# Performance work log

Measured on AMD Instinct MI355X. Metric: run time of the kernel, lower is better.

Reference implementation:

```python
import jax, jax.numpy as jnp
import numpy as np
from jax import lax

T, B, V, N = 128, 256, 256, 1024


def setup_inputs() -> dict:
    key = jax.random.key(0)
    k1, k2, k3, k4 = jax.random.split(key, 4)
    inputs = jax.random.uniform(k1, (T, B, V), dtype=jnp.float32)
    labels = jax.random.uniform(k2, (T * B, V), dtype=jnp.float32)
    weights = jax.random.normal(k3, (V + N, N), dtype=jnp.float32) * 0.1
    bias = jnp.zeros((N,), dtype=jnp.float32)
    output_weights = jax.random.normal(k4, (N, V), dtype=jnp.float32) * 0.1
    output_bias = jnp.zeros((V,), dtype=jnp.float32)
    return {
        "inputs": inputs,
        "labels": labels,
        "weights": weights,
        "bias": bias,
        "output_weights": output_weights,
        "output_bias": output_bias,
    }


def reference(inputs, labels, weights, bias, output_weights, output_bias):
    t, b, v = inputs.shape
    n = weights.shape[1]
    # split concat-matmul into x@Wx + h@Wh (same math as concat([x,h]) @ W)
    w_x = weights[:v]   # [V, N]
    w_h = weights[v:]   # [N, N]

    def step(h, x):
        h_new = jnp.tanh(x @ w_x + h @ w_h + bias)
        return h_new, h_new

    h0 = jnp.zeros((b, n), dtype=inputs.dtype)
    _, outputs = lax.scan(step, h0, inputs)          # [T, B, N]
    outputs = outputs.reshape(t * b, n)              # concat over time
    logits = outputs @ output_weights + output_bias  # [T*B, V]
    # softmax_cross_entropy_with_logits (soft labels), then mean
    log_p = jax.nn.log_softmax(logits, axis=-1)
    loss = jnp.mean(-jnp.sum(labels * log_p, axis=-1))
    return loss
```

## Files before the change

kernel.cpp:

```cpp
#include <hip/hip_runtime.h>
#include <math.h>

typedef __bf16 bf16;
typedef __attribute__((ext_vector_type(4))) __bf16 bf16x4;
typedef __attribute__((ext_vector_type(8))) __bf16 bf16x8;
typedef __attribute__((ext_vector_type(4))) float f32x4;

#define T_STEPS 128
#define B_SZ    256
#define V_SZ    256
#define N_SZ    1024
#define NROWS   (T_STEPS * B_SZ)
#define RSTR    68
#define LSTR    17
#define NGRP    16
#define NCB     16

__device__ __forceinline__ float fast_tanh(float x) {
    float e = __expf(2.0f * x);
    return 1.0f - 2.0f / (e + 1.0f);
}

__global__ void k_convert(const float* __restrict__ src, bf16* __restrict__ dst, int n) {
    int i = (blockIdx.x * blockDim.x + threadIdx.x) * 4;
    if (i < n) {
        float4 v = *(const float4*)(src + i);
        bf16x4 o;
        o.x = (bf16)v.x; o.y = (bf16)v.y; o.z = (bf16)v.z; o.w = (bf16)v.w;
        *(bf16x4*)(dst + i) = o;
    }
}

__global__ void k_transpose_cvt(const float* __restrict__ src, bf16* __restrict__ dst,
                                int R, int C) {
    __shared__ float tile[32][33];
    int c0 = blockIdx.x * 32;
    int r0 = blockIdx.y * 32;
    int tx = threadIdx.x & 31;
    int ty = threadIdx.x >> 5;
#pragma unroll
    for (int i = 0; i < 32; i += 8)
        tile[ty + i][tx] = src[(size_t)(r0 + ty + i) * C + c0 + tx];
    __syncthreads();
#pragma unroll
    for (int i = 0; i < 32; i += 8)
        dst[(size_t)(c0 + ty + i) * R + r0 + tx] = (bf16)tile[tx][ty + i];
}

__global__ __launch_bounds__(512, 2) void k_rnn(
    const bf16* __restrict__ Xb,
    const bf16* __restrict__ Wxt,
    const bf16* __restrict__ Wht,
    const bf16* __restrict__ Wot,
    const float* __restrict__ bias,
    bf16* __restrict__ XH,
    unsigned int* __restrict__ Lgu,
    int* __restrict__ cnt)
{
    __shared__ float red[8 * 16 * RSTR];
    __shared__ float lred[8 * 16 * LSTR];
    const int tid  = threadIdx.x;
    const int lane = tid & 63;
    const int w    = tid >> 6;
    const int quad = lane >> 4;
    const int l15  = lane & 15;
    const int g  = blockIdx.x >> 4;
    const int c  = blockIdx.x & 15;
    const int m0 = g * 16;
    const int n0 = c * 64;
    const int k0 = w * 128;
    const int v0 = w * 32;
    int* gcnt = cnt + g * T_STEPS;

    const bf16* Bp = Wht + (size_t)(n0 + l15) * N_SZ + k0 + quad * 8;
    bf16x8 b[4][4];
#pragma unroll
    for (int nt = 0; nt < 4; ++nt)
#pragma unroll
        for (int kc = 0; kc < 4; ++kc)
            b[nt][kc] = *(const bf16x8*)&Bp[(size_t)(nt * 16) * N_SZ + kc * 32];
    bf16x8 bx[4];
#pragma unroll
    for (int nt = 0; nt < 4; ++nt)
        bx[nt] = *(const bf16x8*)&Wxt[(size_t)(n0 + nt * 16 + l15) * V_SZ + v0 + quad * 8];
    bf16x8 bo[4];
#pragma unroll
    for (int kc = 0; kc < 4; ++kc)
        bo[kc] = *(const bf16x8*)&Wot[(size_t)(c * 16 + l15) * N_SZ + k0 + kc * 32 + quad * 8];

    const int orow = tid >> 5;
    const int ocol = (tid & 31) * 2;
    const float bias0 = bias[n0 + ocol];
    const float bias1 = bias[n0 + ocol + 1];
    const int lrow = w * 2 + (lane >> 3);
    const int lvp  = lane & 7;
    unsigned int* XHu = (unsigned int*)XH;
    const f32x4 zz = {0.f, 0.f, 0.f, 0.f};

    {
        bf16x8 ax = *(const bf16x8*)&Xb[(size_t)(m0 + l15) * V_SZ + v0 + quad * 8];
        f32x4 acc[4] = {zz, zz, zz, zz};
#pragma unroll
        for (int nt = 0; nt < 4; ++nt)
            acc[nt] = __builtin_amdgcn_mfma_f32_16x16x32_bf16(ax, bx[nt], acc[nt], 0, 0, 0);
#pragma unroll
        for (int nt = 0; nt < 4; ++nt)
#pragma unroll
            for (int r = 0; r < 4; ++r)
                red[(w * 16 + quad * 4 + r) * RSTR + nt * 16 + l15] = acc[nt][r];
        __syncthreads();
        float s0 = bias0, s1 = bias1;
#pragma unroll
        for (int w2 = 0; w2 < 8; ++w2) {
            float2 v = *(const float2*)&red[(w2 * 16 + orow) * RSTR + ocol];
            s0 += v.x; s1 += v.y;
        }
        bf16 r0 = (bf16)fast_tanh(s0);
        bf16 r1 = (bf16)fast_tanh(s1);
        unsigned int outw = (unsigned int)__builtin_bit_cast(unsigned short, r0)
                          | ((unsigned int)__builtin_bit_cast(unsigned short, r1) << 16);
        size_t oidx = (((size_t)0 * B_SZ + m0 + orow) * N_SZ + n0 + ocol) >> 1;
        __hip_atomic_store(&XHu[oidx], outw, __ATOMIC_RELAXED, __HIP_MEMORY_SCOPE_AGENT);
        asm volatile("s_waitcnt vmcnt(0)" ::: "memory");
        __syncthreads();
        if (tid == 0)
            __hip_atomic_fetch_add(&gcnt[0], 1, __ATOMIC_RELAXED, __HIP_MEMORY_SCOPE_AGENT);
    }

    for (int t = 1; t < T_STEPS; ++t) {
        bf16x8 ax = *(const bf16x8*)&Xb[((size_t)t * B_SZ + m0 + l15) * V_SZ + v0 + quad * 8];

        if (tid == 0) {
            while (__hip_atomic_load(&gcnt[t - 1], __ATOMIC_RELAXED,
                                     __HIP_MEMORY_SCOPE_AGENT) < NCB)
                __builtin_amdgcn_s_sleep(1);
        }
        __syncthreads();

        const bf16* Ap = XH + ((size_t)(t - 1) * B_SZ + m0 + l15) * N_SZ + k0 + quad * 8;
        bf16x8 a[4];
#pragma unroll
        for (int kc = 0; kc < 4; ++kc)
            a[kc] = *(const bf16x8*)&Ap[kc * 32];

        f32x4 acc[4] = {zz, zz, zz, zz};
#pragma unroll
        for (int nt = 0; nt < 4; ++nt)
            acc[nt] = __builtin_amdgcn_mfma_f32_16x16x32_bf16(ax, bx[nt], acc[nt], 0, 0, 0);
#pragma unroll
        for (int kc = 0; kc < 4; ++kc)
#pragma unroll
            for (int nt = 0; nt < 4; ++nt)
                acc[nt] = __builtin_amdgcn_mfma_f32_16x16x32_bf16(a[kc], b[nt][kc],
                                                                  acc[nt], 0, 0, 0);
        f32x4 lacc = zz;
#pragma unroll
        for (int kc = 0; kc < 4; ++kc)
            lacc = __builtin_amdgcn_mfma_f32_16x16x32_bf16(a[kc], bo[kc], lacc, 0, 0, 0);

#pragma unroll
        for (int nt = 0; nt < 4; ++nt)
#pragma unroll
            for (int r = 0; r < 4; ++r)
                red[(w * 16 + quad * 4 + r) * RSTR + nt * 16 + l15] = acc[nt][r];
#pragma unroll
        for (int r = 0; r < 4; ++r)
            lred[(w * 16 + quad * 4 + r) * LSTR + l15] = lacc[r];
        __syncthreads();

        float s0 = bias0, s1 = bias1;
#pragma unroll
        for (int w2 = 0; w2 < 8; ++w2) {
            float2 v = *(const float2*)&red[(w2 * 16 + orow) * RSTR + ocol];
            s0 += v.x; s1 += v.y;
        }
        bf16 r0 = (bf16)fast_tanh(s0);
        bf16 r1 = (bf16)fast_tanh(s1);
        unsigned int outw = (unsigned int)__builtin_bit_cast(unsigned short, r0)
                          | ((unsigned int)__builtin_bit_cast(unsigned short, r1) << 16);
        size_t oidx = (((size_t)t * B_SZ + m0 + orow) * N_SZ + n0 + ocol) >> 1;
        __hip_atomic_store(&XHu[oidx], outw, __ATOMIC_RELAXED, __HIP_MEMORY_SCOPE_AGENT);

        if (lane < 16) {
            float sa = 0.f, sb = 0.f;
#pragma unroll
            for (int w2 = 0; w2 < 8; ++w2) {
                sa += lred[(w2 * 16 + lrow) * LSTR + lvp * 2];
                sb += lred[(w2 * 16 + lrow) * LSTR + lvp * 2 + 1];
            }
            bf16 pa = (bf16)sa, pb = (bf16)sb;
            unsigned int pw = (unsigned int)__builtin_bit_cast(unsigned short, pa)
                            | ((unsigned int)__builtin_bit_cast(unsigned short, pb) << 16);
            Lgu[(((size_t)(t - 1) * 16 + c) * B_SZ + m0 + lrow) * 8 + lvp] = pw;
        }

        asm volatile("s_waitcnt vmcnt(0)" ::: "memory");
        __syncthreads();
        if (tid == 0)
            __hip_atomic_fetch_add(&gcnt[t], 1, __ATOMIC_RELAXED, __HIP_MEMORY_SCOPE_AGENT);
    }

    if (tid == 0) {
        while (__hip_atomic_load(&gcnt[T_STEPS - 1], __ATOMIC_RELAXED,
                                 __HIP_MEMORY_SCOPE_AGENT) < NCB)
            __builtin_amdgcn_s_sleep(1);
    }
    __syncthreads();
    {
        const bf16* Ap = XH + ((size_t)(T_STEPS - 1) * B_SZ + m0 + l15) * N_SZ + k0 + quad * 8;
        bf16x8 a[4];
#pragma unroll
        for (int kc = 0; kc < 4; ++kc)
            a[kc] = *(const bf16x8*)&Ap[kc * 32];
        f32x4 lacc = zz;
#pragma unroll
        for (int kc = 0; kc < 4; ++kc)
            lacc = __builtin_amdgcn_mfma_f32_16x16x32_bf16(a[kc], bo[kc], lacc, 0, 0, 0);
#pragma unroll
        for (int r = 0; r < 4; ++r)
            lred[(w * 16 + quad * 4 + r) * LSTR + l15] = lacc[r];
        __syncthreads();
        if (lane < 16) {
            float sa = 0.f, sb = 0.f;
#pragma unroll
            for (int w2 = 0; w2 < 8; ++w2) {
                sa += lred[(w2 * 16 + lrow) * LSTR + lvp * 2];
                sb += lred[(w2 * 16 + lrow) * LSTR + lvp * 2 + 1];
            }
            bf16 pa = (bf16)sa, pb = (bf16)sb;
            unsigned int pw = (unsigned int)__builtin_bit_cast(unsigned short, pa)
                            | ((unsigned int)__builtin_bit_cast(unsigned short, pb) << 16);
            Lgu[(((size_t)(T_STEPS - 1) * 16 + c) * B_SZ + m0 + lrow) * 8 + lvp] = pw;
        }
    }
}

__global__ __launch_bounds__(256) void k_lred(
    const bf16* __restrict__ Lg,
    const float* __restrict__ labels,
    const float* __restrict__ ob,
    float* __restrict__ out)
{
    __shared__ float bt[4];
    const int tid  = threadIdx.x;
    const int lane = tid & 63;
    const int w    = tid >> 6;
    const int cs   = lane >> 2;
    const int vi   = (lane & 3) * 4;
    const float4 ob4 = *(const float4*)&ob[cs * 16 + vi];

    float wtot = 0.f;
    for (int i = 0; i < 32; ++i) {
        int row  = blockIdx.x * 128 + w * 32 + i;
        int p    = row >> 8;
        int brow = row & 255;
        bf16x4 lv = *(const bf16x4*)&Lg[(((size_t)p * 16 + cs) * B_SZ + brow) * 16 + vi];
        float l0 = (float)lv.x + ob4.x;
        float l1 = (float)lv.y + ob4.y;
        float l2 = (float)lv.z + ob4.z;
        float l3 = (float)lv.w + ob4.w;
        float mx = fmaxf(fmaxf(l0, l1), fmaxf(l2, l3));
#pragma unroll
        for (int s = 1; s < 64; s <<= 1)
            mx = fmaxf(mx, __shfl_xor(mx, s, 64));
        float sume = __expf(l0 - mx) + __expf(l1 - mx) + __expf(l2 - mx) + __expf(l3 - mx);
        const float4 lb = *(const float4*)&labels[(size_t)row * V_SZ + cs * 16 + vi];
        float labs = lb.x + lb.y + lb.z + lb.w;
        float labv = lb.x * l0 + lb.y * l1 + lb.z * l2 + lb.w * l3;
#pragma unroll
        for (int s = 1; s < 64; s <<= 1) {
            sume += __shfl_xor(sume, s, 64);
            labs += __shfl_xor(labs, s, 64);
            labv += __shfl_xor(labv, s, 64);
        }
        float lse = mx + __logf(sume);
        wtot += labs * lse - labv;
    }
    if (lane == 0) bt[w] = wtot;
    __syncthreads();
    if (tid == 0)
        atomicAdd(out, (bt[0] + bt[1] + bt[2] + bt[3]) * (1.0f / (float)NROWS));
}

extern "C" void kernel_launch(void* const* d_in, const int* in_sizes, int n_in,
                              void* d_out, int out_size, void* d_ws, size_t ws_size,
                              hipStream_t stream)
{
    const float* inputs  = (const float*)d_in[0];
    const float* labels  = (const float*)d_in[1];
    const float* weights = (const float*)d_in[2];
    const float* bias    = (const float*)d_in[3];
    const float* out_w   = (const float*)d_in[4];
    const float* out_b   = (const float*)d_in[5];
    float* out = (float*)d_out;

    char* ws = (char*)d_ws;
    bf16* XH  = (bf16*)ws;  ws += (size_t)NROWS * N_SZ * 2;
    bf16* Xb  = (bf16*)ws;  ws += (size_t)NROWS * V_SZ * 2;
    bf16* Lg  = (bf16*)ws;  ws += (size_t)NROWS * V_SZ * 2;
    bf16* Wxt = (bf16*)ws;  ws += (size_t)N_SZ * V_SZ * 2;
    bf16* Wht = (bf16*)ws;  ws += (size_t)N_SZ * N_SZ * 2;
    bf16* Wot = (bf16*)ws;  ws += (size_t)V_SZ * N_SZ * 2;
    int*  cnt = (int*)ws;   ws += (size_t)NGRP * T_STEPS * 4;

    hipMemsetAsync(out, 0, sizeof(float), stream);
    hipMemsetAsync(cnt, 0, (size_t)NGRP * T_STEPS * 4, stream);

    k_convert<<<dim3(NROWS * V_SZ / 1024), 256, 0, stream>>>(inputs, Xb, NROWS * V_SZ);
    k_transpose_cvt<<<dim3(N_SZ / 32, V_SZ / 32), 256, 0, stream>>>(weights, Wxt, V_SZ, N_SZ);
    k_transpose_cvt<<<dim3(N_SZ / 32, N_SZ / 32), 256, 0, stream>>>(
        weights + (size_t)V_SZ * N_SZ, Wht, N_SZ, N_SZ);
    k_transpose_cvt<<<dim3(V_SZ / 32, N_SZ / 32), 256, 0, stream>>>(out_w, Wot, N_SZ, V_SZ);

    k_rnn<<<dim3(NGRP * NCB), 512, 0, stream>>>(Xb, Wxt, Wht, Wot, bias, XH,
                                                (unsigned int*)Lg, cnt);

    k_lred<<<dim3(NROWS / 128), 256, 0, stream>>>(Lg, labels, out_b, out);
}
```

Measured before the change: 504.0 us.

## Repartition RNN blocks to pair batch groups with narrower column slices

Each block now handles two 16-row batch groups and a 32-column slice of the hidden state, which halves the recurrent weight registers per block while keeping 256 blocks. The output-projection work is split between two half-blocks, and each half writes a partial logit buffer that the loss kernel sums. The wait on the previous step moves to the end of each iteration, so the loss-partial reduction overlaps the spin. In exchange each block now waits on two counters with 32 arrivals each, and the workspace for logits doubles.

```diff
diff --git a/kernel.cpp b/kernel.cpp
--- a/kernel.cpp
+++ b/kernel.cpp
@@ -11,10 +11,10 @@
 #define V_SZ    256
 #define N_SZ    1024
 #define NROWS   (T_STEPS * B_SZ)
-#define RSTR    68
-#define LSTR    17
+#define RST     36
+#define LST     17
 #define NGRP    16
-#define NCB     16
+#define NCB2    32
 
 __device__ __forceinline__ float fast_tanh(float x) {
     float e = __expf(2.0f * x);
@@ -57,181 +57,197 @@
     unsigned int* __restrict__ Lgu,
     int* __restrict__ cnt)
 {
-    __shared__ float red[8 * 16 * RSTR];
-    __shared__ float lred[8 * 16 * LSTR];
+    __shared__ float red0[8 * 16 * RST];
+    __shared__ float red1[8 * 16 * RST];
+    __shared__ float lred0[4 * 16 * LST];
+    __shared__ float lred1[4 * 16 * LST];
     const int tid  = threadIdx.x;
     const int lane = tid & 63;
     const int w    = tid >> 6;
     const int quad = lane >> 4;
     const int l15  = lane & 15;
-    const int g  = blockIdx.x >> 4;
-    const int c  = blockIdx.x & 15;
-    const int m0 = g * 16;
-    const int n0 = c * 64;
+    const int gp = blockIdx.x >> 5;
+    const int c  = blockIdx.x & 31;
+    const int g0 = gp * 2, g1 = gp * 2 + 1;
+    const int m00 = g0 * 16, m01 = g1 * 16;
+    const int n0 = c * 32;
     const int k0 = w * 128;
     const int v0 = w * 32;
-    int* gcnt = cnt + g * T_STEPS;
+    const int h  = c & 1;
+    const int s  = c >> 1;
+    const bool lossw = ((w >> 2) == h);
+    const int wl = w & 3;
+    int* gc0 = cnt + g0 * T_STEPS;
+    int* gc1 = cnt + g1 * T_STEPS;
 
     const bf16* Bp = Wht + (size_t)(n0 + l15) * N_SZ + k0 + quad * 8;
-    bf16x8 b[4][4];
-#pragma unroll
-    for (int nt = 0; nt < 4; ++nt)
+    bf16x8 b[2][4];
+#pragma unroll
+    for (int nt = 0; nt < 2; ++nt)
 #pragma unroll
         for (int kc = 0; kc < 4; ++kc)
             b[nt][kc] = *(const bf16x8*)&Bp[(size_t)(nt * 16) * N_SZ + kc * 32];
-    bf16x8 bx[4];
-#pragma unroll
-    for (int nt = 0; nt < 4; ++nt)
+    bf16x8 bx[2];
+#pragma unroll
+    for (int nt = 0; nt < 2; ++nt)
         bx[nt] = *(const bf16x8*)&Wxt[(size_t)(n0 + nt * 16 + l15) * V_SZ + v0 + quad * 8];
     bf16x8 bo[4];
-#pragma unroll
-    for (int kc = 0; kc < 4; ++kc)
-        bo[kc] = *(const bf16x8*)&Wot[(size_t)(c * 16 + l15) * N_SZ + k0 + kc * 32 + quad * 8];
-
-    const int orow = tid >> 5;
-    const int ocol = (tid & 31) * 2;
+    if (lossw) {
+#pragma unroll
+        for (int kc = 0; kc < 4; ++kc)
+            bo[kc] = *(const bf16x8*)&Wot[(size_t)(s * 16 + l15) * N_SZ + k0 + kc * 32 + quad * 8];
+    }
+
+    const int  et   = tid & 255;
+    const int  orow = et >> 4;
+    const int  ocol = (et & 15) * 2;
+    const int  mg   = (tid >= 256) ? m01 : m00;
+    float* redp = (tid >= 256) ? red1 : red0;
     const float bias0 = bias[n0 + ocol];
     const float bias1 = bias[n0 + ocol + 1];
-    const int lrow = w * 2 + (lane >> 3);
-    const int lvp  = lane & 7;
+    const bool lactive = (tid >= 128 && tid < 256) || (tid >= 384);
+    const int  lt   = (tid >= 384) ? (tid - 384) : (tid - 128);
+    const int  lrow = lt >> 3, lvp = lt & 7;
+    float* lredp = (tid >= 384) ? lred1 : lred0;
+    const int  lm  = (tid >= 384) ? m01 : m00;
     unsigned int* XHu = (unsigned int*)XH;
     const f32x4 zz = {0.f, 0.f, 0.f, 0.f};
 
     {
-        bf16x8 ax = *(const bf16x8*)&Xb[(size_t)(m0 + l15) * V_SZ + v0 + quad * 8];
-        f32x4 acc[4] = {zz, zz, zz, zz};
-#pragma unroll
-        for (int nt = 0; nt < 4; ++nt)
-            acc[nt] = __builtin_amdgcn_mfma_f32_16x16x32_bf16(ax, bx[nt], acc[nt], 0, 0, 0);
-#pragma unroll
-        for (int nt = 0; nt < 4; ++nt)
-#pragma unroll
-            for (int r = 0; r < 4; ++r)
-                red[(w * 16 + quad * 4 + r) * RSTR + nt * 16 + l15] = acc[nt][r];
+        bf16x8 ax0 = *(const bf16x8*)&Xb[(size_t)(m00 + l15) * V_SZ + v0 + quad * 8];
+        bf16x8 ax1 = *(const bf16x8*)&Xb[(size_t)(m01 + l15) * V_SZ + v0 + quad * 8];
+        f32x4 acc0[2] = {zz, zz}, acc1[2] = {zz, zz};
+#pragma unroll
+        for (int nt = 0; nt < 2; ++nt) {
+            acc0[nt] = __builtin_amdgcn_mfma_f32_16x16x32_bf16(ax0, bx[nt], acc0[nt], 0, 0, 0);
+            acc1[nt] = __builtin_amdgcn_mfma_f32_16x16x32_bf16(ax1, bx[nt], acc1[nt], 0, 0, 0);
+        }
+#pragma unroll
+        for (int nt = 0; nt < 2; ++nt)
+#pragma unroll
+            for (int r = 0; r < 4; ++r) {
+                red0[(w * 16 + quad * 4 + r) * RST + nt * 16 + l15] = acc0[nt][r];
+                red1[(w * 16 + quad * 4 + r) * RST + nt * 16 + l15] = acc1[nt][r];
+            }
         __syncthreads();
         float s0 = bias0, s1 = bias1;
 #pragma unroll
         for (int w2 = 0; w2 < 8; ++w2) {
-            float2 v = *(const float2*)&red[(w2 * 16 + orow) * RSTR + ocol];
+            float2 v = *(const float2*)&redp[(w2 * 16 + orow) * RST + ocol];
             s0 += v.x; s1 += v.y;
         }
         bf16 r0 = (bf16)fast_tanh(s0);
         bf16 r1 = (bf16)fast_tanh(s1);
         unsigned int outw = (unsigned int)__builtin_bit_cast(unsigned short, r0)
                           | ((unsigned int)__builtin_bit_cast(unsigned short, r1) << 16);
-        size_t oidx = (((size_t)0 * B_SZ + m0 + orow) * N_SZ + n0 + ocol) >> 1;
+        size_t oidx = (((size_t)mg + orow) * N_SZ + n0 + ocol) >> 1;
         __hip_atomic_store(&XHu[oidx], outw, __ATOMIC_RELAXED, __HIP_MEMORY_SCOPE_AGENT);
         asm volatile("s_waitcnt vmcnt(0)" ::: "memory");
         __syncthreads();
-        if (tid == 0)
-            __hip_atomic_fetch_add(&gcnt[0], 1, __ATOMIC_RELAXED, __HIP_MEMORY_SCOPE_AGENT);
-    }
-
-    for (int t = 1; t < T_STEPS; ++t) {
-        bf16x8 ax = *(const bf16x8*)&Xb[((size_t)t * B_SZ + m0 + l15) * V_SZ + v0 + quad * 8];
-
         if (tid == 0) {
-            while (__hip_atomic_load(&gcnt[t - 1], __ATOMIC_RELAXED,
-                                     __HIP_MEMORY_SCOPE_AGENT) < NCB)
+            __hip_atomic_fetch_add(&gc0[0], 1, __ATOMIC_RELAXED, __HIP_MEMORY_SCOPE_AGENT);
+            __hip_atomic_fetch_add(&gc1[0], 1, __ATOMIC_RELAXED, __HIP_MEMORY_SCOPE_AGENT);
+            while (__hip_atomic_load(&gc0[0], __ATOMIC_RELAXED, __HIP_MEMORY_SCOPE_AGENT) < NCB2)
                 __builtin_amdgcn_s_sleep(1);
-        }
-        __syncthreads();
-
-        const bf16* Ap = XH + ((size_t)(t - 1) * B_SZ + m0 + l15) * N_SZ + k0 + quad * 8;
-        bf16x8 a[4];
-#pragma unroll
-        for (int kc = 0; kc < 4; ++kc)
-            a[kc] = *(const bf16x8*)&Ap[kc * 32];
-
-        f32x4 acc[4] = {zz, zz, zz, zz};
-#pragma unroll
-        for (int nt = 0; nt < 4; ++nt)
-            acc[nt] = __builtin_amdgcn_mfma_f32_16x16x32_bf16(ax, bx[nt], acc[nt], 0, 0, 0);
-#pragma unroll
-        for (int kc = 0; kc < 4; ++kc)
-#pragma unroll
-            for (int nt = 0; nt < 4; ++nt)
-                acc[nt] = __builtin_amdgcn_mfma_f32_16x16x32_bf16(a[kc], b[nt][kc],
-                                                                  acc[nt], 0, 0, 0);
-        f32x4 lacc = zz;
-#pragma unroll
-        for (int kc = 0; kc < 4; ++kc)
-            lacc = __builtin_amdgcn_mfma_f32_16x16x32_bf16(a[kc], bo[kc], lacc, 0, 0, 0);
-
-#pragma unroll
-        for (int nt = 0; nt < 4; ++nt)
-#pragma unroll
-            for (int r = 0; r < 4; ++r)
-                red[(w * 16 + quad * 4 + r) * RSTR + nt * 16 + l15] = acc[nt][r];
-#pragma unroll
-        for (int r = 0; r < 4; ++r)
-            lred[(w * 16 + quad * 4 + r) * LSTR + l15] = lacc[r];
-        __syncthreads();
-
-        float s0 = bias0, s1 = bias1;
-#pragma unroll
-        for (int w2 = 0; w2 < 8; ++w2) {
-            float2 v = *(const float2*)&red[(w2 * 16 + orow) * RSTR + ocol];
-            s0 += v.x; s1 += v.y;
-        }
-        bf16 r0 = (bf16)fast_tanh(s0);
-        bf16 r1 = (bf16)fast_tanh(s1);
-        unsigned int outw = (unsigned int)__builtin_bit_cast(unsigned short, r0)
-                          | ((unsigned int)__builtin_bit_cast(unsigned short, r1) << 16);
-        size_t oidx = (((size_t)t * B_SZ + m0 + orow) * N_SZ + n0 + ocol) >> 1;
-        __hip_atomic_store(&XHu[oidx], outw, __ATOMIC_RELAXED, __HIP_MEMORY_SCOPE_AGENT);
-
-        if (lane < 16) {
+            while (__hip_atomic_load(&gc1[0], __ATOMIC_RELAXED, __HIP_MEMORY_SCOPE_AGENT) < NCB2)
+                __builtin_amdgcn_s_sleep(1);
+        }
+        __syncthreads();
+    }
+
+    for (int t = 1; t <= T_STEPS; ++t) {
+        const bool do_step = (t < T_STEPS);
+
+        bf16x8 ax0, ax1;
+        if (do_step) {
+            ax0 = *(const bf16x8*)&Xb[((size_t)t * B_SZ + m00 + l15) * V_SZ + v0 + quad * 8];
+            ax1 = *(const bf16x8*)&Xb[((size_t)t * B_SZ + m01 + l15) * V_SZ + v0 + quad * 8];
+        }
+
+        const bf16* Ap0 = XH + ((size_t)(t - 1) * B_SZ + m00 + l15) * N_SZ + k0 + quad * 8;
+        const bf16* Ap1 = XH + ((size_t)(t - 1) * B_SZ + m01 + l15) * N_SZ + k0 + quad * 8;
+        bf16x8 a0[4], a1[4];
+#pragma unroll
+        for (int kc = 0; kc < 4; ++kc) {
+            a0[kc] = *(const bf16x8*)&Ap0[kc * 32];
+            a1[kc] = *(const bf16x8*)&Ap1[kc * 32];
+        }
+
+        if (do_step) {
+            f32x4 acc0[2] = {zz, zz}, acc1[2] = {zz, zz};
+#pragma unroll
+            for (int nt = 0; nt < 2; ++nt) {
+                acc0[nt] = __builtin_amdgcn_mfma_f32_16x16x32_bf16(ax0, bx[nt], acc0[nt], 0, 0, 0);
+                acc1[nt] = __builtin_amdgcn_mfma_f32_16x16x32_bf16(ax1, bx[nt], acc1[nt], 0, 0, 0);
+            }
+#pragma unroll
+            for (int kc = 0; kc < 4; ++kc)
+#pragma unroll
+                for (int nt = 0; nt < 2; ++nt) {
+                    acc0[nt] = __builtin_amdgcn_mfma_f32_16x16x32_bf16(a0[kc], b[nt][kc], acc0[nt], 0, 0, 0);
+                    acc1[nt] = __builtin_amdgcn_mfma_f32_16x16x32_bf16(a1[kc], b[nt][kc], acc1[nt], 0, 0, 0);
+                }
+#pragma unroll
+            for (int nt = 0; nt < 2; ++nt)
+#pragma unroll
+                for (int r = 0; r < 4; ++r) {
+                    red0[(w * 16 + quad * 4 + r) * RST + nt * 16 + l15] = acc0[nt][r];
+                    red1[(w * 16 + quad * 4 + r) * RST + nt * 16 + l15] = acc1[nt][r];
+                }
+        }
+        if (lossw) {
+            f32x4 lacc0 = zz, lacc1 = zz;
+#pragma unroll
+            for (int kc = 0; kc < 4; ++kc) {
+                lacc0 = __builtin_amdgcn_mfma_f32_16x16x32_bf16(a0[kc], bo[kc], lacc0, 0, 0, 0);
+                lacc1 = __builtin_amdgcn_mfma_f32_16x16x32_bf16(a1[kc], bo[kc], lacc1, 0, 0, 0);
+            }
+#pragma unroll
+            for (int r = 0; r < 4; ++r) {
+                lred0[(wl * 16 + quad * 4 + r) * LST + l15] = lacc0[r];
+                lred1[(wl * 16 + quad * 4 + r) * LST + l15] = lacc1[r];
+            }
+        }
+        __syncthreads();
+
+        if (do_step) {
+            float s0 = bias0, s1 = bias1;
+#pragma unroll
+            for (int w2 = 0; w2 < 8; ++w2) {
+                float2 v = *(const float2*)&redp[(w2 * 16 + orow) * RST + ocol];
+                s0 += v.x; s1 += v.y;
+            }
+            bf16 r0 = (bf16)fast_tanh(s0);
+            bf16 r1 = (bf16)fast_tanh(s1);
+            unsigned int outw = (unsigned int)__builtin_bit_cast(unsigned short, r0)
+                              | ((unsigned int)__builtin_bit_cast(unsigned short, r1) << 16);
+            size_t oidx = (((size_t)t * B_SZ + mg + orow) * N_SZ + n0 + ocol) >> 1;
+            __hip_atomic_store(&XHu[oidx], outw, __ATOMIC_RELAXED, __HIP_MEMORY_SCOPE_AGENT);
+            asm volatile("s_waitcnt vmcnt(0)" ::: "memory");
+        }
+        __syncthreads();
+
+        if (tid == 0 && do_step) {
+            __hip_atomic_fetch_add(&gc0[t], 1, __ATOMIC_RELAXED, __HIP_MEMORY_SCOPE_AGENT);
+            __hip_atomic_fetch_add(&gc1[t], 1, __ATOMIC_RELAXED, __HIP_MEMORY_SCOPE_AGENT);
+            while (__hip_atomic_load(&gc0[t], __ATOMIC_RELAXED, __HIP_MEMORY_SCOPE_AGENT) < NCB2)
+                __builtin_amdgcn_s_sleep(1);
+            while (__hip_atomic_load(&gc1[t], __ATOMIC_RELAXED, __HIP_MEMORY_SCOPE_AGENT) < NCB2)
+                __builtin_amdgcn_s_sleep(1);
+        }
+        if (lactive) {
             float sa = 0.f, sb = 0.f;
 #pragma unroll
-            for (int w2 = 0; w2 < 8; ++w2) {
-                sa += lred[(w2 * 16 + lrow) * LSTR + lvp * 2];
-                sb += lred[(w2 * 16 + lrow) * LSTR + lvp * 2 + 1];
+            for (int w2 = 0; w2 < 4; ++w2) {
+                sa += lredp[(w2 * 16 + lrow) * LST + lvp * 2];
+                sb += lredp[(w2 * 16 + lrow) * LST + lvp * 2 + 1];
             }
             bf16 pa = (bf16)sa, pb = (bf16)sb;
             unsigned int pw = (unsigned int)__builtin_bit_cast(unsigned short, pa)
                             | ((unsigned int)__builtin_bit_cast(unsigned short, pb) << 16);
-            Lgu[(((size_t)(t - 1) * 16 + c) * B_SZ + m0 + lrow) * 8 + lvp] = pw;
-        }
-
-        asm volatile("s_waitcnt vmcnt(0)" ::: "memory");
-        __syncthreads();
-        if (tid == 0)
-            __hip_atomic_fetch_add(&gcnt[t], 1, __ATOMIC_RELAXED, __HIP_MEMORY_SCOPE_AGENT);
-    }
-
-    if (tid == 0) {
-        while (__hip_atomic_load(&gcnt[T_STEPS - 1], __ATOMIC_RELAXED,
-                                 __HIP_MEMORY_SCOPE_AGENT) < NCB)
-            __builtin_amdgcn_s_sleep(1);
-    }
-    __syncthreads();
-    {
-        const bf16* Ap = XH + ((size_t)(T_STEPS - 1) * B_SZ + m0 + l15) * N_SZ + k0 + quad * 8;
-        bf16x8 a[4];
-#pragma unroll
-        for (int kc = 0; kc < 4; ++kc)
-            a[kc] = *(const bf16x8*)&Ap[kc * 32];
-        f32x4 lacc = zz;
-#pragma unroll
-        for (int kc = 0; kc < 4; ++kc)
-            lacc = __builtin_amdgcn_mfma_f32_16x16x32_bf16(a[kc], bo[kc], lacc, 0, 0, 0);
-#pragma unroll
-        for (int r = 0; r < 4; ++r)
-            lred[(w * 16 + quad * 4 + r) * LSTR + l15] = lacc[r];
-        __syncthreads();
-        if (lane < 16) {
-            float sa = 0.f, sb = 0.f;
-#pragma unroll
-            for (int w2 = 0; w2 < 8; ++w2) {
-                sa += lred[(w2 * 16 + lrow) * LSTR + lvp * 2];
-                sb += lred[(w2 * 16 + lrow) * LSTR + lvp * 2 + 1];
-            }
-            bf16 pa = (bf16)sa, pb = (bf16)sb;
-            unsigned int pw = (unsigned int)__builtin_bit_cast(unsigned short, pa)
-                            | ((unsigned int)__builtin_bit_cast(unsigned short, pb) << 16);
-            Lgu[(((size_t)(T_STEPS - 1) * 16 + c) * B_SZ + m0 + lrow) * 8 + lvp] = pw;
-        }
+            Lgu[((((size_t)h * T_STEPS + (t - 1)) * 16 + s) * B_SZ + lm + lrow) * 8 + lvp] = pw;
+        }
+        __syncthreads();
     }
 }
 
@@ -242,6 +258,7 @@
     float* __restrict__ out)
 {
     __shared__ float bt[4];
+    const size_t HS = (size_t)NROWS * V_SZ;
     const int tid  = threadIdx.x;
     const int lane = tid & 63;
     const int w    = tid >> 6;
@@ -254,24 +271,26 @@
         int row  = blockIdx.x * 128 + w * 32 + i;
         int p    = row >> 8;
         int brow = row & 255;
-        bf16x4 lv = *(const bf16x4*)&Lg[(((size_t)p * 16 + cs) * B_SZ + brow) * 16 + vi];
-        float l0 = (float)lv.x + ob4.x;
-        float l1 = (float)lv.y + ob4.y;
-        float l2 = (float)lv.z + ob4.z;
-        float l3 = (float)lv.w + ob4.w;
+        size_t idx = (((size_t)p * 16 + cs) * B_SZ + brow) * 16 + vi;
+        bf16x4 va = *(const bf16x4*)&Lg[idx];
+        bf16x4 vb = *(const bf16x4*)&Lg[HS + idx];
+        float l0 = (float)va.x + (float)vb.x + ob4.x;
+        float l1 = (float)va.y + (float)vb.y + ob4.y;
+        float l2 = (float)va.z + (float)vb.z + ob4.z;
+        float l3 = (float)va.w + (float)vb.w + ob4.w;
         float mx = fmaxf(fmaxf(l0, l1), fmaxf(l2, l3));
 #pragma unroll
-        for (int s = 1; s < 64; s <<= 1)
-            mx = fmaxf(mx, __shfl_xor(mx, s, 64));
+        for (int sft = 1; sft < 64; sft <<= 1)
+            mx = fmaxf(mx, __shfl_xor(mx, sft, 64));
         float sume = __expf(l0 - mx) + __expf(l1 - mx) + __expf(l2 - mx) + __expf(l3 - mx);
         const float4 lb = *(const float4*)&labels[(size_t)row * V_SZ + cs * 16 + vi];
         float labs = lb.x + lb.y + lb.z + lb.w;
         float labv = lb.x * l0 + lb.y * l1 + lb.z * l2 + lb.w * l3;
 #pragma unroll
-        for (int s = 1; s < 64; s <<= 1) {
-            sume += __shfl_xor(sume, s, 64);
-            labs += __shfl_xor(labs, s, 64);
-            labv += __shfl_xor(labv, s, 64);
+        for (int sft = 1; sft < 64; sft <<= 1) {
+            sume += __shfl_xor(sume, sft, 64);
+            labs += __shfl_xor(labs, sft, 64);
+            labv += __shfl_xor(labv, sft, 64);
         }
         float lse = mx + __logf(sume);
         wtot += labs * lse - labv;
@@ -297,7 +316,7 @@
     char* ws = (char*)d_ws;
     bf16* XH  = (bf16*)ws;  ws += (size_t)NROWS * N_SZ * 2;
     bf16* Xb  = (bf16*)ws;  ws += (size_t)NROWS * V_SZ * 2;
-    bf16* Lg  = (bf16*)ws;  ws += (size_t)NROWS * V_SZ * 2;
+    bf16* Lg  = (bf16*)ws;  ws += (size_t)2 * NROWS * V_SZ * 2;
     bf16* Wxt = (bf16*)ws;  ws += (size_t)N_SZ * V_SZ * 2;
     bf16* Wht = (bf16*)ws;  ws += (size_t)N_SZ * N_SZ * 2;
     bf16* Wot = (bf16*)ws;  ws += (size_t)V_SZ * N_SZ * 2;
@@ -312,8 +331,8 @@
         weights + (size_t)V_SZ * N_SZ, Wht, N_SZ, N_SZ);
     k_transpose_cvt<<<dim3(V_SZ / 32, N_SZ / 32), 256, 0, stream>>>(out_w, Wot, N_SZ, V_SZ);
 
-    k_rnn<<<dim3(NGRP * NCB), 512, 0, stream>>>(Xb, Wxt, Wht, Wot, bias, XH,
-                                                (unsigned int*)Lg, cnt);
+    k_rnn<<<dim3(256), 512, 0, stream>>>(Xb, Wxt, Wht, Wot, bias, XH,
+                                         (unsigned int*)Lg, cnt);
 
     k_lred<<<dim3(NROWS / 128), 256, 0, stream>>>(Lg, labels, out_b, out);
 }
```

After: 730.7 us. +45.0%, slower.

## Replace per-step block barrier with per-wave flag waits and fuse input conversion

Applied to the files above, without the earlier changes.

Replaces the per-group atomic counter and block-wide barrier with per-producer flags, so each wave waits only for the two column blocks whose hidden-state slice it reads. This lets waves start their matmul independently instead of waiting for the whole group. Input fp32-to-bf16 conversion moves into the RNN kernel, removing a separate conversion pass and its workspace traffic. The logit layout also becomes row-major so the loss kernel reads contiguous rows. Risks are a larger flag buffer to memset and busier polling from many waves.

```diff
diff --git a/kernel.cpp b/kernel.cpp
--- a/kernel.cpp
+++ b/kernel.cpp
@@ -15,20 +15,19 @@
 #define LSTR    17
 #define NGRP    16
 #define NCB     16
+#define FIDX(g,t,c) ((((g) * T_STEPS + (t)) * 16 + (c)) * 32)
+#define FLG_INTS    (NGRP * T_STEPS * 16 * 32)
 
 __device__ __forceinline__ float fast_tanh(float x) {
     float e = __expf(2.0f * x);
     return 1.0f - 2.0f / (e + 1.0f);
 }
 
-__global__ void k_convert(const float* __restrict__ src, bf16* __restrict__ dst, int n) {
-    int i = (blockIdx.x * blockDim.x + threadIdx.x) * 4;
-    if (i < n) {
-        float4 v = *(const float4*)(src + i);
-        bf16x4 o;
-        o.x = (bf16)v.x; o.y = (bf16)v.y; o.z = (bf16)v.z; o.w = (bf16)v.w;
-        *(bf16x4*)(dst + i) = o;
-    }
+__device__ __forceinline__ bf16x8 cvt_bf16x8(float4 a, float4 b) {
+    bf16x8 r;
+    r[0] = (bf16)a.x; r[1] = (bf16)a.y; r[2] = (bf16)a.z; r[3] = (bf16)a.w;
+    r[4] = (bf16)b.x; r[5] = (bf16)b.y; r[6] = (bf16)b.z; r[7] = (bf16)b.w;
+    return r;
 }
 
 __global__ void k_transpose_cvt(const float* __restrict__ src, bf16* __restrict__ dst,
@@ -48,14 +47,14 @@
 }
 
 __global__ __launch_bounds__(512, 2) void k_rnn(
-    const bf16* __restrict__ Xb,
+    const float* __restrict__ Xf,
     const bf16* __restrict__ Wxt,
     const bf16* __restrict__ Wht,
     const bf16* __restrict__ Wot,
     const float* __restrict__ bias,
     bf16* __restrict__ XH,
     unsigned int* __restrict__ Lgu,
-    int* __restrict__ cnt)
+    int* __restrict__ flg)
 {
     __shared__ float red[8 * 16 * RSTR];
     __shared__ float lred[8 * 16 * LSTR];
@@ -70,7 +69,6 @@
     const int n0 = c * 64;
     const int k0 = w * 128;
     const int v0 = w * 32;
-    int* gcnt = cnt + g * T_STEPS;
 
     const bf16* Bp = Wht + (size_t)(n0 + l15) * N_SZ + k0 + quad * 8;
     bf16x8 b[4][4];
@@ -96,9 +94,12 @@
     const int lvp  = lane & 7;
     unsigned int* XHu = (unsigned int*)XH;
     const f32x4 zz = {0.f, 0.f, 0.f, 0.f};
+    const size_t xin = (size_t)(m0 + l15) * V_SZ + v0 + quad * 8;
 
     {
-        bf16x8 ax = *(const bf16x8*)&Xb[(size_t)(m0 + l15) * V_SZ + v0 + quad * 8];
+        float4 f0 = *(const float4*)&Xf[xin];
+        float4 f1 = *(const float4*)&Xf[xin + 4];
+        bf16x8 ax = cvt_bf16x8(f0, f1);
         f32x4 acc[4] = {zz, zz, zz, zz};
 #pragma unroll
         for (int nt = 0; nt < 4; ++nt)
@@ -119,23 +120,28 @@
         bf16 r1 = (bf16)fast_tanh(s1);
         unsigned int outw = (unsigned int)__builtin_bit_cast(unsigned short, r0)
                           | ((unsigned int)__builtin_bit_cast(unsigned short, r1) << 16);
-        size_t oidx = (((size_t)0 * B_SZ + m0 + orow) * N_SZ + n0 + ocol) >> 1;
+        size_t oidx = (((size_t)m0 + orow) * N_SZ + n0 + ocol) >> 1;
         __hip_atomic_store(&XHu[oidx], outw, __ATOMIC_RELAXED, __HIP_MEMORY_SCOPE_AGENT);
         asm volatile("s_waitcnt vmcnt(0)" ::: "memory");
         __syncthreads();
         if (tid == 0)
-            __hip_atomic_fetch_add(&gcnt[0], 1, __ATOMIC_RELAXED, __HIP_MEMORY_SCOPE_AGENT);
+            __hip_atomic_store(&flg[FIDX(g, 0, c)], 1,
+                               __ATOMIC_RELAXED, __HIP_MEMORY_SCOPE_AGENT);
     }
 
     for (int t = 1; t < T_STEPS; ++t) {
-        bf16x8 ax = *(const bf16x8*)&Xb[((size_t)t * B_SZ + m0 + l15) * V_SZ + v0 + quad * 8];
-
-        if (tid == 0) {
-            while (__hip_atomic_load(&gcnt[t - 1], __ATOMIC_RELAXED,
-                                     __HIP_MEMORY_SCOPE_AGENT) < NCB)
+        float4 f0 = *(const float4*)&Xf[(size_t)t * B_SZ * V_SZ + xin];
+        float4 f1 = *(const float4*)&Xf[(size_t)t * B_SZ * V_SZ + xin + 4];
+
+        if (lane == 0) {
+            const int* fp0 = &flg[FIDX(g, t - 1, 2 * w)];
+            while (__hip_atomic_load(fp0, __ATOMIC_RELAXED, __HIP_MEMORY_SCOPE_AGENT) == 0)
                 __builtin_amdgcn_s_sleep(1);
-        }
-        __syncthreads();
+            const int* fp1 = &flg[FIDX(g, t - 1, 2 * w + 1)];
+            while (__hip_atomic_load(fp1, __ATOMIC_RELAXED, __HIP_MEMORY_SCOPE_AGENT) == 0)
+                __builtin_amdgcn_s_sleep(1);
+        }
+        asm volatile("" ::: "memory");
 
         const bf16* Ap = XH + ((size_t)(t - 1) * B_SZ + m0 + l15) * N_SZ + k0 + quad * 8;
         bf16x8 a[4];
@@ -143,6 +149,7 @@
         for (int kc = 0; kc < 4; ++kc)
             a[kc] = *(const bf16x8*)&Ap[kc * 32];
 
+        bf16x8 ax = cvt_bf16x8(f0, f1);
         f32x4 acc[4] = {zz, zz, zz, zz};
 #pragma unroll
         for (int nt = 0; nt < 4; ++nt)
@@ -191,21 +198,25 @@
             bf16 pa = (bf16)sa, pb = (bf16)sb;
             unsigned int pw = (unsigned int)__builtin_bit_cast(unsigned short, pa)
                             | ((unsigned int)__builtin_bit_cast(unsigned short, pb) << 16);
-            Lgu[(((size_t)(t - 1) * 16 + c) * B_SZ + m0 + lrow) * 8 + lvp] = pw;
+            Lgu[((size_t)(t - 1) * B_SZ + m0 + lrow) * 128 + c * 8 + lvp] = pw;
         }
 
         asm volatile("s_waitcnt vmcnt(0)" ::: "memory");
         __syncthreads();
         if (tid == 0)
-            __hip_atomic_fetch_add(&gcnt[t], 1, __ATOMIC_RELAXED, __HIP_MEMORY_SCOPE_AGENT);
-    }
-
-    if (tid == 0) {
-        while (__hip_atomic_load(&gcnt[T_STEPS - 1], __ATOMIC_RELAXED,
-                                 __HIP_MEMORY_SCOPE_AGENT) < NCB)
+            __hip_atomic_store(&flg[FIDX(g, t, c)], 1,
+                               __ATOMIC_RELAXED, __HIP_MEMORY_SCOPE_AGENT);
+    }
+
+    if (lane == 0) {
+        const int* fp0 = &flg[FIDX(g, T_STEPS - 1, 2 * w)];
+        while (__hip_atomic_load(fp0, __ATOMIC_RELAXED, __HIP_MEMORY_SCOPE_AGENT) == 0)
             __builtin_amdgcn_s_sleep(1);
-    }
-    __syncthreads();
+        const int* fp1 = &flg[FIDX(g, T_STEPS - 1, 2 * w + 1)];
+        while (__hip_atomic_load(fp1, __ATOMIC_RELAXED, __HIP_MEMORY_SCOPE_AGENT) == 0)
+            __builtin_amdgcn_s_sleep(1);
+    }
+    asm volatile("" ::: "memory");
     {
         const bf16* Ap = XH + ((size_t)(T_STEPS - 1) * B_SZ + m0 + l15) * N_SZ + k0 + quad * 8;
         bf16x8 a[4];
@@ -230,7 +241,7 @@
             bf16 pa = (bf16)sa, pb = (bf16)sb;
             unsigned int pw = (unsigned int)__builtin_bit_cast(unsigned short, pa)
                             | ((unsigned int)__builtin_bit_cast(unsigned short, pb) << 16);
-            Lgu[(((size_t)(T_STEPS - 1) * 16 + c) * B_SZ + m0 + lrow) * 8 + lvp] = pw;
+            Lgu[((size_t)(T_STEPS - 1) * B_SZ + m0 + lrow) * 128 + c * 8 + lvp] = pw;
         }
     }
 }
@@ -245,33 +256,29 @@
     const int tid  = threadIdx.x;
     const int lane = tid & 63;
     const int w    = tid >> 6;
-    const int cs   = lane >> 2;
-    const int vi   = (lane & 3) * 4;
-    const float4 ob4 = *(const float4*)&ob[cs * 16 + vi];
+    const float4 ob4 = *(const float4*)&ob[lane * 4];
 
     float wtot = 0.f;
     for (int i = 0; i < 32; ++i) {
-        int row  = blockIdx.x * 128 + w * 32 + i;
-        int p    = row >> 8;
-        int brow = row & 255;
-        bf16x4 lv = *(const bf16x4*)&Lg[(((size_t)p * 16 + cs) * B_SZ + brow) * 16 + vi];
+        int row = blockIdx.x * 128 + w * 32 + i;
+        bf16x4 lv = *(const bf16x4*)&Lg[(size_t)row * V_SZ + lane * 4];
         float l0 = (float)lv.x + ob4.x;
         float l1 = (float)lv.y + ob4.y;
         float l2 = (float)lv.z + ob4.z;
         float l3 = (float)lv.w + ob4.w;
         float mx = fmaxf(fmaxf(l0, l1), fmaxf(l2, l3));
 #pragma unroll
-        for (int s = 1; s < 64; s <<= 1)
-            mx = fmaxf(mx, __shfl_xor(mx, s, 64));
+        for (int sft = 1; sft < 64; sft <<= 1)
+            mx = fmaxf(mx, __shfl_xor(mx, sft, 64));
         float sume = __expf(l0 - mx) + __expf(l1 - mx) + __expf(l2 - mx) + __expf(l3 - mx);
-        const float4 lb = *(const float4*)&labels[(size_t)row * V_SZ + cs * 16 + vi];
+        const float4 lb = *(const float4*)&labels[(size_t)row * V_SZ + lane * 4];
         float labs = lb.x + lb.y + lb.z + lb.w;
         float labv = lb.x * l0 + lb.y * l1 + lb.z * l2 + lb.w * l3;
 #pragma unroll
-        for (int s = 1; s < 64; s <<= 1) {
-            sume += __shfl_xor(sume, s, 64);
-            labs += __shfl_xor(labs, s, 64);
-            labv += __shfl_xor(labv, s, 64);
+        for (int sft = 1; sft < 64; sft <<= 1) {
+            sume += __shfl_xor(sume, sft, 64);
+            labs += __shfl_xor(labs, sft, 64);
+            labv += __shfl_xor(labv, sft, 64);
         }
         float lse = mx + __logf(sume);
         wtot += labs * lse - labv;
@@ -296,24 +303,22 @@
 
     char* ws = (char*)d_ws;
     bf16* XH  = (bf16*)ws;  ws += (size_t)NROWS * N_SZ * 2;
-    bf16* Xb  = (bf16*)ws;  ws += (size_t)NROWS * V_SZ * 2;
     bf16* Lg  = (bf16*)ws;  ws += (size_t)NROWS * V_SZ * 2;
     bf16* Wxt = (bf16*)ws;  ws += (size_t)N_SZ * V_SZ * 2;
     bf16* Wht = (bf16*)ws;  ws += (size_t)N_SZ * N_SZ * 2;
     bf16* Wot = (bf16*)ws;  ws += (size_t)V_SZ * N_SZ * 2;
-    int*  cnt = (int*)ws;   ws += (size_t)NGRP * T_STEPS * 4;
+    int*  flg = (int*)ws;   ws += (size_t)FLG_INTS * 4;
 
     hipMemsetAsync(out, 0, sizeof(float), stream);
-    hipMemsetAsync(cnt, 0, (size_t)NGRP * T_STEPS * 4, stream);
-
-    k_convert<<<dim3(NROWS * V_SZ / 1024), 256, 0, stream>>>(inputs, Xb, NROWS * V_SZ);
+    hipMemsetAsync(flg, 0, (size_t)FLG_INTS * 4, stream);
+
     k_transpose_cvt<<<dim3(N_SZ / 32, V_SZ / 32), 256, 0, stream>>>(weights, Wxt, V_SZ, N_SZ);
     k_transpose_cvt<<<dim3(N_SZ / 32, N_SZ / 32), 256, 0, stream>>>(
         weights + (size_t)V_SZ * N_SZ, Wht, N_SZ, N_SZ);
     k_transpose_cvt<<<dim3(V_SZ / 32, N_SZ / 32), 256, 0, stream>>>(out_w, Wot, N_SZ, V_SZ);
 
-    k_rnn<<<dim3(NGRP * NCB), 512, 0, stream>>>(Xb, Wxt, Wht, Wot, bias, XH,
-                                                (unsigned int*)Lg, cnt);
+    k_rnn<<<dim3(NGRP * NCB), 512, 0, stream>>>(inputs, Wxt, Wht, Wot, bias, XH,
+                                                (unsigned int*)Lg, flg);
 
     k_lred<<<dim3(NROWS / 128), 256, 0, stream>>>(Lg, labels, out_b, out);
 }
```

New measurement: 539.3 us. +7.0%, slower.

## Fuse input bf16 conversion into RNN kernel and merge weight transposes

Applied to the files above, without the earlier changes.

Drops the separate pass that converted the input sequence to bf16 in global memory. The RNN kernel now loads the fp32 inputs directly, prefetching them before the step barrier and converting in registers. The three weight transpose launches are merged into a single prep kernel with block-index dispatch. This cuts one full read/write pass over the inputs and two launches, at the cost of doubling the per-step input load bytes inside the latency-critical recurrent loop.

```diff
diff --git a/kernel.cpp b/kernel.cpp
--- a/kernel.cpp
+++ b/kernel.cpp
@@ -21,34 +21,48 @@
     return 1.0f - 2.0f / (e + 1.0f);
 }
 
-__global__ void k_convert(const float* __restrict__ src, bf16* __restrict__ dst, int n) {
-    int i = (blockIdx.x * blockDim.x + threadIdx.x) * 4;
-    if (i < n) {
-        float4 v = *(const float4*)(src + i);
-        bf16x4 o;
-        o.x = (bf16)v.x; o.y = (bf16)v.y; o.z = (bf16)v.z; o.w = (bf16)v.w;
-        *(bf16x4*)(dst + i) = o;
-    }
-}
-
-__global__ void k_transpose_cvt(const float* __restrict__ src, bf16* __restrict__ dst,
-                                int R, int C) {
+__device__ __forceinline__ bf16x8 cvt_bf16x8(float4 a, float4 b) {
+    bf16x8 r;
+    r[0] = (bf16)a.x; r[1] = (bf16)a.y; r[2] = (bf16)a.z; r[3] = (bf16)a.w;
+    r[4] = (bf16)b.x; r[5] = (bf16)b.y; r[6] = (bf16)b.z; r[7] = (bf16)b.w;
+    return r;
+}
+
+__global__ __launch_bounds__(256) void k_prep(
+    const float* __restrict__ weights,
+    const float* __restrict__ out_w,
+    bf16* __restrict__ Wxt,
+    bf16* __restrict__ Wht,
+    bf16* __restrict__ Wot)
+{
     __shared__ float tile[32][33];
-    int c0 = blockIdx.x * 32;
-    int r0 = blockIdx.y * 32;
+    int id = blockIdx.x;
+    const float* src; bf16* dst; int R, C, tr, tc;
+    if (id < 256) {
+        src = weights; dst = Wxt; R = V_SZ; C = N_SZ;
+        tr = (id & 7) * 32; tc = (id >> 3) * 32;
+    } else if (id < 1280) {
+        id -= 256;
+        src = weights + (size_t)V_SZ * N_SZ; dst = Wht; R = N_SZ; C = N_SZ;
+        tr = (id & 31) * 32; tc = (id >> 5) * 32;
+    } else {
+        id -= 1280;
+        src = out_w; dst = Wot; R = N_SZ; C = V_SZ;
+        tr = (id & 31) * 32; tc = (id >> 5) * 32;
+    }
     int tx = threadIdx.x & 31;
     int ty = threadIdx.x >> 5;
 #pragma unroll
     for (int i = 0; i < 32; i += 8)
-        tile[ty + i][tx] = src[(size_t)(r0 + ty + i) * C + c0 + tx];
+        tile[ty + i][tx] = src[(size_t)(tr + ty + i) * C + tc + tx];
     __syncthreads();
 #pragma unroll
     for (int i = 0; i < 32; i += 8)
-        dst[(size_t)(c0 + ty + i) * R + r0 + tx] = (bf16)tile[tx][ty + i];
+        dst[(size_t)(tc + ty + i) * R + tr + tx] = (bf16)tile[tx][ty + i];
 }
 
 __global__ __launch_bounds__(512, 2) void k_rnn(
-    const bf16* __restrict__ Xb,
+    const float* __restrict__ Xf,
     const bf16* __restrict__ Wxt,
     const bf16* __restrict__ Wht,
     const bf16* __restrict__ Wot,
@@ -96,9 +110,12 @@
     const int lvp  = lane & 7;
     unsigned int* XHu = (unsigned int*)XH;
     const f32x4 zz = {0.f, 0.f, 0.f, 0.f};
+    const size_t xin = (size_t)(m0 + l15) * V_SZ + v0 + quad * 8;
 
     {
-        bf16x8 ax = *(const bf16x8*)&Xb[(size_t)(m0 + l15) * V_SZ + v0 + quad * 8];
+        float4 f0 = *(const float4*)&Xf[xin];
+        float4 f1 = *(const float4*)&Xf[xin + 4];
+        bf16x8 ax = cvt_bf16x8(f0, f1);
         f32x4 acc[4] = {zz, zz, zz, zz};
 #pragma unroll
         for (int nt = 0; nt < 4; ++nt)
@@ -119,7 +136,7 @@
         bf16 r1 = (bf16)fast_tanh(s1);
         unsigned int outw = (unsigned int)__builtin_bit_cast(unsigned short, r0)
                           | ((unsigned int)__builtin_bit_cast(unsigned short, r1) << 16);
-        size_t oidx = (((size_t)0 * B_SZ + m0 + orow) * N_SZ + n0 + ocol) >> 1;
+        size_t oidx = (((size_t)m0 + orow) * N_SZ + n0 + ocol) >> 1;
         __hip_atomic_store(&XHu[oidx], outw, __ATOMIC_RELAXED, __HIP_MEMORY_SCOPE_AGENT);
         asm volatile("s_waitcnt vmcnt(0)" ::: "memory");
         __syncthreads();
@@ -128,7 +145,8 @@
     }
 
     for (int t = 1; t < T_STEPS; ++t) {
-        bf16x8 ax = *(const bf16x8*)&Xb[((size_t)t * B_SZ + m0 + l15) * V_SZ + v0 + quad * 8];
+        float4 f0 = *(const float4*)&Xf[(size_t)t * B_SZ * V_SZ + xin];
+        float4 f1 = *(const float4*)&Xf[(size_t)t * B_SZ * V_SZ + xin + 4];
 
         if (tid == 0) {
             while (__hip_atomic_load(&gcnt[t - 1], __ATOMIC_RELAXED,
@@ -143,6 +161,7 @@
         for (int kc = 0; kc < 4; ++kc)
             a[kc] = *(const bf16x8*)&Ap[kc * 32];
 
+        bf16x8 ax = cvt_bf16x8(f0, f1);
         f32x4 acc[4] = {zz, zz, zz, zz};
 #pragma unroll
         for (int nt = 0; nt < 4; ++nt)
@@ -261,17 +280,17 @@
         float l3 = (float)lv.w + ob4.w;
         float mx = fmaxf(fmaxf(l0, l1), fmaxf(l2, l3));
 #pragma unroll
-        for (int s = 1; s < 64; s <<= 1)
-            mx = fmaxf(mx, __shfl_xor(mx, s, 64));
+        for (int sft = 1; sft < 64; sft <<= 1)
+            mx = fmaxf(mx, __shfl_xor(mx, sft, 64));
         float sume = __expf(l0 - mx) + __expf(l1 - mx) + __expf(l2 - mx) + __expf(l3 - mx);
         const float4 lb = *(const float4*)&labels[(size_t)row * V_SZ + cs * 16 + vi];
         float labs = lb.x + lb.y + lb.z + lb.w;
         float labv = lb.x * l0 + lb.y * l1 + lb.z * l2 + lb.w * l3;
 #pragma unroll
-        for (int s = 1; s < 64; s <<= 1) {
-            sume += __shfl_xor(sume, s, 64);
-            labs += __shfl_xor(labs, s, 64);
-            labv += __shfl_xor(labv, s, 64);
+        for (int sft = 1; sft < 64; sft <<= 1) {
+            sume += __shfl_xor(sume, sft, 64);
+            labs += __shfl_xor(labs, sft, 64);
+            labv += __shfl_xor(labv, sft, 64);
         }
         float lse = mx + __logf(sume);
         wtot += labs * lse - labv;
@@ -296,7 +315,6 @@
 
     char* ws = (char*)d_ws;
     bf16* XH  = (bf16*)ws;  ws += (size_t)NROWS * N_SZ * 2;
-    bf16* Xb  = (bf16*)ws;  ws += (size_t)NROWS * V_SZ * 2;
     bf16* Lg  = (bf16*)ws;  ws += (size_t)NROWS * V_SZ * 2;
     bf16* Wxt = (bf16*)ws;  ws += (size_t)N_SZ * V_SZ * 2;
     bf16* Wht = (bf16*)ws;  ws += (size_t)N_SZ * N_SZ * 2;
@@ -306,13 +324,9 @@
     hipMemsetAsync(out, 0, sizeof(float), stream);
     hipMemsetAsync(cnt, 0, (size_t)NGRP * T_STEPS * 4, stream);
 
-    k_convert<<<dim3(NROWS * V_SZ / 1024), 256, 0, stream>>>(inputs, Xb, NROWS * V_SZ);
-    k_transpose_cvt<<<dim3(N_SZ / 32, V_SZ / 32), 256, 0, stream>>>(weights, Wxt, V_SZ, N_SZ);
-    k_transpose_cvt<<<dim3(N_SZ / 32, N_SZ / 32), 256, 0, stream>>>(
-        weights + (size_t)V_SZ * N_SZ, Wht, N_SZ, N_SZ);
-    k_transpose_cvt<<<dim3(V_SZ / 32, N_SZ / 32), 256, 0, stream>>>(out_w, Wot, N_SZ, V_SZ);
-
-    k_rnn<<<dim3(NGRP * NCB), 512, 0, stream>>>(Xb, Wxt, Wht, Wot, bias, XH,
+    k_prep<<<dim3(1536), 256, 0, stream>>>(weights, out_w, Wxt, Wht, Wot);
+
+    k_rnn<<<dim3(NGRP * NCB), 512, 0, stream>>>(inputs, Wxt, Wht, Wot, bias, XH,
                                                 (unsigned int*)Lg, cnt);
 
     k_lred<<<dim3(NROWS / 128), 256, 0, stream>>>(Lg, labels, out_b, out);
```

New measurement: 498.0 us. About the same (-1.2%).
